# Optimization experiments

Hardware: AMD Instinct MI355X
Metric: run time of the kernel (lower is better)

The kernel has to match this reference:

```python
import jax, jax.numpy as jnp
import numpy as np

B, D_IN, D_OUT, Q_DIM = 8192, 400, 100, 10


def setup_inputs() -> dict:
    key = jax.random.key(0)
    kx, kw = jax.random.split(key)
    X = jax.random.normal(kx, (B, D_IN, Q_DIM), dtype=jnp.float32)
    # FRMap weight: randn(d_out, d_in) / sqrt(d_in)
    W = jax.random.normal(kw, (D_OUT, D_IN), dtype=jnp.float32) / (D_IN ** 0.5)
    return {"X": X, "W": W}


def reference(X, W):
    # FRMap: Y[b] = W @ X[b]  -> (B, d_out, q)
    Y = jnp.einsum('oi,biq->boq', W, X)
    # ReOrth: reduced QR of each tall-skinny (d_out, q) matrix, keep Q
    Q, _ = jnp.linalg.qr(Y, mode='reduced')  # (B, d_out, q)
    return Q
```

## Files before the change

kernel.cpp:

```cpp
#include <hip/hip_runtime.h>
#include <math.h>

#define BATCHES 8192
#define D_IN    400
#define D_OUT   100
#define QD      10
#define KT      64
#define NKT     7
#define MTILES  7
#define WFSZ    (NKT * MTILES * 2 * 64 * 8)
#define XB      648
#define NW      4

using bf16x8 = __attribute__((ext_vector_type(8))) short;
using f32x4  = __attribute__((ext_vector_type(4))) float;

template <int CTRL>
__device__ __forceinline__ float dpp_add(float x) {
  int s = __builtin_amdgcn_update_dpp(0, __builtin_bit_cast(int, x),
                                      CTRL, 0xF, 0xF, true);
  return x + __builtin_bit_cast(float, s);
}

__device__ __forceinline__ float wsum64(float x) {
  x = dpp_add<0x111>(x);
  x = dpp_add<0x112>(x);
  x = dpp_add<0x114>(x);
  x = dpp_add<0x118>(x);
  x = dpp_add<0x142>(x);
  x = dpp_add<0x143>(x);
  return __builtin_bit_cast(float,
      __builtin_amdgcn_readlane(__builtin_bit_cast(int, x), 63));
}

__device__ __forceinline__ float lane_bcast(float x, int lane) {
  return __builtin_bit_cast(float,
      __builtin_amdgcn_readlane(__builtin_bit_cast(int, x), lane));
}

__global__ __launch_bounds__(256) void wprep_kernel(const float* __restrict__ W,
                                                    short* __restrict__ wfh,
                                                    short* __restrict__ wfl) {
  const int e = blockIdx.x * 256 + threadIdx.x;
  if (e >= WFSZ) return;
  const int j = e & 7, lane = (e >> 3) & 63, ks = (e >> 9) & 1, mtkt = e >> 10;
  const int kt = mtkt / MTILES, mt = mtkt - kt * MTILES;
  const int o = mt * 16 + (lane & 15);
  const int k = kt * KT + ks * 32 + (lane >> 4) * 8 + j;
  const float w = (o < D_OUT && k < D_IN) ? W[o * D_IN + k] : 0.f;
  __bf16 h = (__bf16)w;
  float hf = (float)h;
  __bf16 l = (__bf16)(w - hf);
  wfh[e] = __builtin_bit_cast(short, h);
  wfl[e] = __builtin_bit_cast(short, l);
}


__device__ __forceinline__ void qr_and_store(const f32x4* acc, float* stg,
                                             float* dst, int lane, int col,
                                             int quad) {
  if (col < QD) {
    #pragma unroll
    for (int mt = 0; mt < MTILES; ++mt)
      #pragma unroll
      for (int rr = 0; rr < 4; ++rr) {
        const int o = mt * 16 + quad * 4 + rr;
        if (o < D_OUT) stg[o * QD + col] = acc[mt][rr];
      }
  }
  const int r = lane;
  float a0[QD], a1[QD];
  #pragma unroll
  for (int q = 0; q < QD; ++q) a0[q] = stg[r * QD + q];
  const bool has1 = (r + 64) < D_OUT;
  #pragma unroll
  for (int q = 0; q < QD; ++q) a1[q] = has1 ? stg[(r + 64) * QD + q] : 0.f;

  float v0[QD], v1[QD], tau[QD];
  #pragma unroll
  for (int j = 0; j < QD; ++j) {
    float cj0  = (r >= j) ? a0[j] : 0.f;
    float part = cj0 * cj0 + a1[j] * a1[j];
    float sig  = wsum64(part);
    float alpha = lane_bcast(a0[j], j);
    float nrm  = sqrtf(sig);
    float beta = (alpha >= 0.f) ? -nrm : nrm;
    float tj   = (nrm > 0.f) ? (beta - alpha) / beta : 0.f;
    float inv  = (nrm > 0.f) ? 1.f / (alpha - beta) : 0.f;
    tau[j] = tj;
    v0[j]  = (r == j) ? 1.f : ((r > j) ? a0[j] * inv : 0.f);
    v1[j]  = a1[j] * inv;
    #pragma unroll
    for (int k = j + 1; k < QD; ++k) {
      float p = v0[j] * a0[k] + v1[j] * a1[k];
      float s = wsum64(p) * tj;
      a0[k] -= s * v0[j];
      a1[k] -= s * v1[j];
    }
  }
  float q0[QD], q1[QD];
  #pragma unroll
  for (int c = 0; c < QD; ++c) { q0[c] = (r == c) ? 1.f : 0.f; q1[c] = 0.f; }
  #pragma unroll
  for (int j = QD - 1; j >= 0; --j) {
    #pragma unroll
    for (int c = j; c < QD; ++c) {
      float p = v0[j] * q0[c] + v1[j] * q1[c];
      float s = wsum64(p) * tau[j];
      q0[c] -= s * v0[j];
      q1[c] -= s * v1[j];
    }
  }
  #pragma unroll
  for (int c = 0; c < QD; ++c) stg[r * QD + c] = q0[c];
  if (has1) {
    #pragma unroll
    for (int c = 0; c < QD; ++c) stg[(r + 64) * QD + c] = q1[c];
  }
  const float4* src = (const float4*)stg;
  float4* d4 = (float4*)dst;
  #pragma unroll
  for (int u = r; u < (D_OUT * QD) / 4; u += 64) d4[u] = src[u];
}

__global__ __launch_bounds__(256, 3) void fused_kernel(const float* __restrict__ X,
                                                       const short* __restrict__ wfh,
                                                       const short* __restrict__ wfl,
                                                       float* __restrict__ out) {
  __shared__ float xstg[NW * 2 * XB];
  const int tid  = threadIdx.x;
  const int lane = tid & 63;
  const int wv   = __builtin_amdgcn_readfirstlane(tid >> 6);
  const long b0  = (long)blockIdx.x * (NW * 2) + wv * 2;
  float* xs = xstg + wv * (2 * XB);
  const int col = lane & 15, quad = lane >> 4;

  f32x4 acc0[MTILES], acc1[MTILES];
  #pragma unroll
  for (int t = 0; t < MTILES; ++t) {
    acc0[t] = (f32x4){0.f, 0.f, 0.f, 0.f};
    acc1[t] = (f32x4){0.f, 0.f, 0.f, 0.f};
  }

  float4 pre[5];
  #pragma unroll
  for (int u = 0; u < 5; ++u) {
    const int idx = lane + u * 64;
    const int bsel = idx >= 160 ? 1 : 0;
    const int within = idx - bsel * 160;
    pre[u] = *(const float4*)(X + (b0 + bsel) * (long)(D_IN * QD) + within * 4);
  }

  #pragma unroll 1
  for (int kt = 0; kt < NKT; ++kt) {
    const int k0 = kt * KT;
    #pragma unroll
    for (int u = 0; u < 5; ++u) {
      const int idx = lane + u * 64;
      const int bsel = idx >= 160 ? 1 : 0;
      const int within = idx - bsel * 160;
      *(float4*)&xs[bsel * XB + within * 4] = pre[u];
    }
    if (kt + 1 < NKT) {
      const int nk0 = k0 + KT;
      const int vf4 = (nk0 + KT <= D_IN) ? 160 : ((D_IN - nk0) * QD) / 4;
      #pragma unroll
      for (int u = 0; u < 5; ++u) {
        const int idx = lane + u * 64;
        const int bsel = idx >= 160 ? 1 : 0;
        const int within = idx - bsel * 160;
        float4 v = {0.f, 0.f, 0.f, 0.f};
        if (within < vf4)
          v = *(const float4*)(X + (b0 + bsel) * (long)(D_IN * QD) + nk0 * QD + within * 4);
        pre[u] = v;
      }
    }
    const short* wh_kt = wfh + (long)kt * (MTILES * 2 * 64 * 8);
    const short* wl_kt = wfl + (long)kt * (MTILES * 2 * 64 * 8);
    #pragma unroll
    for (int ks = 0; ks < 2; ++ks) {
      bf16x8 b0h, b0l, b1h, b1l;
      #pragma unroll
      for (int m = 0; m < 8; ++m) {
        const int fo = (ks * 32 + quad * 8 + m) * QD + col;
        float x0 = xs[fo];
        float x1 = xs[XB + fo];
        __bf16 h0 = (__bf16)x0; float f0 = (float)h0; __bf16 g0 = (__bf16)(x0 - f0);
        __bf16 h1 = (__bf16)x1; float f1 = (float)h1; __bf16 g1 = (__bf16)(x1 - f1);
        b0h[m] = __builtin_bit_cast(short, h0); b0l[m] = __builtin_bit_cast(short, g0);
        b1h[m] = __builtin_bit_cast(short, h1); b1l[m] = __builtin_bit_cast(short, g1);
      }
      #pragma unroll
      for (int mt = 0; mt < MTILES; ++mt) {
        const int ao = ((mt * 2 + ks) * 64 + lane) * 8;
        bf16x8 ah = *(const bf16x8*)(wh_kt + ao);
        bf16x8 al = *(const bf16x8*)(wl_kt + ao);
        acc0[mt] = __builtin_amdgcn_mfma_f32_16x16x32_bf16(ah, b0h, acc0[mt], 0, 0, 0);
        acc0[mt] = __builtin_amdgcn_mfma_f32_16x16x32_bf16(al, b0h, acc0[mt], 0, 0, 0);
        acc0[mt] = __builtin_amdgcn_mfma_f32_16x16x32_bf16(ah, b0l, acc0[mt], 0, 0, 0);
        acc1[mt] = __builtin_amdgcn_mfma_f32_16x16x32_bf16(ah, b1h, acc1[mt], 0, 0, 0);
        acc1[mt] = __builtin_amdgcn_mfma_f32_16x16x32_bf16(al, b1h, acc1[mt], 0, 0, 0);
        acc1[mt] = __builtin_amdgcn_mfma_f32_16x16x32_bf16(ah, b1l, acc1[mt], 0, 0, 0);
      }
    }
  }

  qr_and_store(acc0, xs, out + b0 * (long)(D_OUT * QD), lane, col, quad);
  qr_and_store(acc1, xs, out + (b0 + 1) * (long)(D_OUT * QD), lane, col, quad);
}

extern "C" void kernel_launch(void* const* d_in, const int* in_sizes, int n_in,
                              void* d_out, int out_size, void* d_ws, size_t ws_size,
                              hipStream_t stream) {
  const float* X = (const float*)d_in[0];
  const float* W = (const float*)d_in[1];
  float* out = (float*)d_out;
  short* wfh = (short*)d_ws;
  short* wfl = wfh + WFSZ;
  hipLaunchKernelGGL(wprep_kernel, dim3((WFSZ + 255) / 256), dim3(256), 0, stream,
                     W, wfh, wfl);
  hipLaunchKernelGGL(fused_kernel, dim3(BATCHES / (NW * 2)), dim3(256), 0, stream,
                     X, wfh, wfl, out);
}
```

Measured before the change: 272.5 us.

## Process one batch per wave and use fast rcp/sqrt in Householder QR

```diff
diff --git a/kernel.cpp b/kernel.cpp
--- a/kernel.cpp
+++ b/kernel.cpp
@@ -9,7 +9,7 @@
 #define NKT     7
 #define MTILES  7
 #define WFSZ    (NKT * MTILES * 2 * 64 * 8)
-#define XB      648
+#define XR      1008
 #define NW      4
 
 using bf16x8 = __attribute__((ext_vector_type(8))) short;
@@ -83,10 +83,13 @@
     float part = cj0 * cj0 + a1[j] * a1[j];
     float sig  = wsum64(part);
     float alpha = lane_bcast(a0[j], j);
-    float nrm  = sqrtf(sig);
-    float beta = (alpha >= 0.f) ? -nrm : nrm;
-    float tj   = (nrm > 0.f) ? (beta - alpha) / beta : 0.f;
-    float inv  = (nrm > 0.f) ? 1.f / (alpha - beta) : 0.f;
+    float nrm  = __builtin_amdgcn_sqrtf(sig);
+    float aab  = fabsf(alpha);
+    float rn   = __builtin_amdgcn_rcpf(nrm);
+    float rd   = __builtin_amdgcn_rcpf(aab + nrm);
+    float sgn  = (alpha >= 0.f) ? 1.f : -1.f;
+    float tj   = (sig > 0.f) ? (1.f + aab * rn) : 0.f;
+    float inv  = (sig > 0.f) ? sgn * rd : 0.f;
     tau[j] = tj;
     v0[j]  = (r == j) ? 1.f : ((r > j) ? a0[j] * inv : 0.f);
     v1[j]  = a1[j] * inv;
@@ -123,55 +126,48 @@
   for (int u = r; u < (D_OUT * QD) / 4; u += 64) d4[u] = src[u];
 }
 
-__global__ __launch_bounds__(256, 3) void fused_kernel(const float* __restrict__ X,
+__global__ __launch_bounds__(256, 4) void fused_kernel(const float* __restrict__ X,
                                                        const short* __restrict__ wfh,
                                                        const short* __restrict__ wfl,
                                                        float* __restrict__ out) {
-  __shared__ float xstg[NW * 2 * XB];
+  __shared__ float xstg[NW * XR];
   const int tid  = threadIdx.x;
   const int lane = tid & 63;
   const int wv   = __builtin_amdgcn_readfirstlane(tid >> 6);
-  const long b0  = (long)blockIdx.x * (NW * 2) + wv * 2;
-  float* xs = xstg + wv * (2 * XB);
+  const long b   = (long)blockIdx.x * NW + wv;
+  float* xs = xstg + wv * XR;
   const int col = lane & 15, quad = lane >> 4;
 
-  f32x4 acc0[MTILES], acc1[MTILES];
-  #pragma unroll
-  for (int t = 0; t < MTILES; ++t) {
-    acc0[t] = (f32x4){0.f, 0.f, 0.f, 0.f};
-    acc1[t] = (f32x4){0.f, 0.f, 0.f, 0.f};
-  }
-
-  float4 pre[5];
-  #pragma unroll
-  for (int u = 0; u < 5; ++u) {
+  f32x4 acc[MTILES];
+  #pragma unroll
+  for (int t = 0; t < MTILES; ++t) acc[t] = (f32x4){0.f, 0.f, 0.f, 0.f};
+
+  float4 pre[3];
+  #pragma unroll
+  for (int u = 0; u < 3; ++u) {
     const int idx = lane + u * 64;
-    const int bsel = idx >= 160 ? 1 : 0;
-    const int within = idx - bsel * 160;
-    pre[u] = *(const float4*)(X + (b0 + bsel) * (long)(D_IN * QD) + within * 4);
+    pre[u] = (float4){0.f, 0.f, 0.f, 0.f};
+    if (idx < 160)
+      pre[u] = *(const float4*)(X + b * (long)(D_IN * QD) + idx * 4);
   }
 
   #pragma unroll 1
   for (int kt = 0; kt < NKT; ++kt) {
     const int k0 = kt * KT;
     #pragma unroll
-    for (int u = 0; u < 5; ++u) {
+    for (int u = 0; u < 3; ++u) {
       const int idx = lane + u * 64;
-      const int bsel = idx >= 160 ? 1 : 0;
-      const int within = idx - bsel * 160;
-      *(float4*)&xs[bsel * XB + within * 4] = pre[u];
+      if (idx < 160) *(float4*)&xs[idx * 4] = pre[u];
     }
     if (kt + 1 < NKT) {
       const int nk0 = k0 + KT;
       const int vf4 = (nk0 + KT <= D_IN) ? 160 : ((D_IN - nk0) * QD) / 4;
       #pragma unroll
-      for (int u = 0; u < 5; ++u) {
+      for (int u = 0; u < 3; ++u) {
         const int idx = lane + u * 64;
-        const int bsel = idx >= 160 ? 1 : 0;
-        const int within = idx - bsel * 160;
         float4 v = {0.f, 0.f, 0.f, 0.f};
-        if (within < vf4)
-          v = *(const float4*)(X + (b0 + bsel) * (long)(D_IN * QD) + nk0 * QD + within * 4);
+        if (idx < vf4)
+          v = *(const float4*)(X + b * (long)(D_IN * QD) + nk0 * QD + idx * 4);
         pre[u] = v;
       }
     }
@@ -179,34 +175,28 @@
     const short* wl_kt = wfl + (long)kt * (MTILES * 2 * 64 * 8);
     #pragma unroll
     for (int ks = 0; ks < 2; ++ks) {
-      bf16x8 b0h, b0l, b1h, b1l;
+      bf16x8 bh, bl;
       #pragma unroll
       for (int m = 0; m < 8; ++m) {
         const int fo = (ks * 32 + quad * 8 + m) * QD + col;
         float x0 = xs[fo];
-        float x1 = xs[XB + fo];
         __bf16 h0 = (__bf16)x0; float f0 = (float)h0; __bf16 g0 = (__bf16)(x0 - f0);
-        __bf16 h1 = (__bf16)x1; float f1 = (float)h1; __bf16 g1 = (__bf16)(x1 - f1);
-        b0h[m] = __builtin_bit_cast(short, h0); b0l[m] = __builtin_bit_cast(short, g0);
-        b1h[m] = __builtin_bit_cast(short, h1); b1l[m] = __builtin_bit_cast(short, g1);
+        bh[m] = __builtin_bit_cast(short, h0);
+        bl[m] = __builtin_bit_cast(short, g0);
       }
       #pragma unroll
       for (int mt = 0; mt < MTILES; ++mt) {
         const int ao = ((mt * 2 + ks) * 64 + lane) * 8;
         bf16x8 ah = *(const bf16x8*)(wh_kt + ao);
         bf16x8 al = *(const bf16x8*)(wl_kt + ao);
-        acc0[mt] = __builtin_amdgcn_mfma_f32_16x16x32_bf16(ah, b0h, acc0[mt], 0, 0, 0);
-        acc0[mt] = __builtin_amdgcn_mfma_f32_16x16x32_bf16(al, b0h, acc0[mt], 0, 0, 0);
-        acc0[mt] = __builtin_amdgcn_mfma_f32_16x16x32_bf16(ah, b0l, acc0[mt], 0, 0, 0);
-        acc1[mt] = __builtin_amdgcn_mfma_f32_16x16x32_bf16(ah, b1h, acc1[mt], 0, 0, 0);
-        acc1[mt] = __builtin_amdgcn_mfma_f32_16x16x32_bf16(al, b1h, acc1[mt], 0, 0, 0);
-        acc1[mt] = __builtin_amdgcn_mfma_f32_16x16x32_bf16(ah, b1l, acc1[mt], 0, 0, 0);
-      }
-    }
-  }
-
-  qr_and_store(acc0, xs, out + b0 * (long)(D_OUT * QD), lane, col, quad);
-  qr_and_store(acc1, xs, out + (b0 + 1) * (long)(D_OUT * QD), lane, col, quad);
+        acc[mt] = __builtin_amdgcn_mfma_f32_16x16x32_bf16(ah, bh, acc[mt], 0, 0, 0);
+        acc[mt] = __builtin_amdgcn_mfma_f32_16x16x32_bf16(al, bh, acc[mt], 0, 0, 0);
+        acc[mt] = __builtin_amdgcn_mfma_f32_16x16x32_bf16(ah, bl, acc[mt], 0, 0, 0);
+      }
+    }
+  }
+
+  qr_and_store(acc, xs, out + b * (long)(D_OUT * QD), lane, col, quad);
 }
 
 extern "C" void kernel_launch(void* const* d_in, const int* in_sizes, int n_in,
@@ -219,6 +209,6 @@
   short* wfl = wfh + WFSZ;
   hipLaunchKernelGGL(wprep_kernel, dim3((WFSZ + 255) / 256), dim3(256), 0, stream,
                      W, wfh, wfl);
-  hipLaunchKernelGGL(fused_kernel, dim3(BATCHES / (NW * 2)), dim3(256), 0, stream,
+  hipLaunchKernelGGL(fused_kernel, dim3(BATCHES / NW), dim3(256), 0, stream,
                      X, wfh, wfl, out);
 }
```

New measurement: 260.6 us. 4.3% less time.

## Stage W fragments in shared memory cooperatively and use fast rcp/sqrt in QR

Applied to the files above, without the earlier changes.

```diff
diff --git a/kernel.cpp b/kernel.cpp
--- a/kernel.cpp
+++ b/kernel.cpp
@@ -11,6 +11,8 @@
 #define WFSZ    (NKT * MTILES * 2 * 64 * 8)
 #define XB      648
 #define NW      4
+#define WCH     512
+#define WHALF   (14 * WCH)
 
 using bf16x8 = __attribute__((ext_vector_type(8))) short;
 using f32x4  = __attribute__((ext_vector_type(4))) float;
@@ -36,6 +38,12 @@
 __device__ __forceinline__ float lane_bcast(float x, int lane) {
   return __builtin_bit_cast(float,
       __builtin_amdgcn_readlane(__builtin_bit_cast(int, x), lane));
+}
+
+__device__ __forceinline__ void lds_barrier() {
+  asm volatile("s_waitcnt lgkmcnt(0)" ::: "memory");
+  __builtin_amdgcn_s_barrier();
+  __builtin_amdgcn_sched_barrier(0);
 }
 
 __global__ __launch_bounds__(256) void wprep_kernel(const float* __restrict__ W,
@@ -55,7 +63,6 @@
   wfl[e] = __builtin_bit_cast(short, l);
 }
 
-
 __device__ __forceinline__ void qr_and_store(const f32x4* acc, float* stg,
                                              float* dst, int lane, int col,
                                              int quad) {
@@ -83,10 +90,13 @@
     float part = cj0 * cj0 + a1[j] * a1[j];
     float sig  = wsum64(part);
     float alpha = lane_bcast(a0[j], j);
-    float nrm  = sqrtf(sig);
-    float beta = (alpha >= 0.f) ? -nrm : nrm;
-    float tj   = (nrm > 0.f) ? (beta - alpha) / beta : 0.f;
-    float inv  = (nrm > 0.f) ? 1.f / (alpha - beta) : 0.f;
+    float nrm  = __builtin_amdgcn_sqrtf(sig);
+    float aab  = fabsf(alpha);
+    float rn   = __builtin_amdgcn_rcpf(nrm);
+    float rd   = __builtin_amdgcn_rcpf(aab + nrm);
+    float sgn  = (alpha >= 0.f) ? 1.f : -1.f;
+    float tj   = (sig > 0.f) ? (1.f + aab * rn) : 0.f;
+    float inv  = (sig > 0.f) ? sgn * rd : 0.f;
     tau[j] = tj;
     v0[j]  = (r == j) ? 1.f : ((r > j) ? a0[j] * inv : 0.f);
     v1[j]  = a1[j] * inv;
@@ -123,11 +133,12 @@
   for (int u = r; u < (D_OUT * QD) / 4; u += 64) d4[u] = src[u];
 }
 
-__global__ __launch_bounds__(256, 3) void fused_kernel(const float* __restrict__ X,
+__global__ __launch_bounds__(256, 4) void fused_kernel(const float* __restrict__ X,
                                                        const short* __restrict__ wfh,
                                                        const short* __restrict__ wfl,
                                                        float* __restrict__ out) {
-  __shared__ float xstg[NW * 2 * XB];
+  __shared__ __align__(16) float xstg[NW * 2 * XB];
+  __shared__ __align__(16) short wtile[WHALF];
   const int tid  = threadIdx.x;
   const int lane = tid & 63;
   const int wv   = __builtin_amdgcn_readfirstlane(tid >> 6);
@@ -142,18 +153,42 @@
     acc1[t] = (f32x4){0.f, 0.f, 0.f, 0.f};
   }
 
+  bf16x8 wst[4];
+  auto wload = [&](int kt, int ks) {
+    #pragma unroll
+    for (int i = 0; i < 4; ++i) {
+      const int c = wv + 4 * i;
+      if (c < 14) {
+        const short* pl = (c < 7) ? wfh : wfl;
+        const int m = (c < 7) ? c : c - 7;
+        wst[i] = *(const bf16x8*)(pl + ((long)(kt * 7 + m) * 2 + ks) * WCH + lane * 8);
+      }
+    }
+  };
+  auto wcommit = [&]() {
+    #pragma unroll
+    for (int i = 0; i < 4; ++i) {
+      const int c = wv + 4 * i;
+      if (c < 14) *(bf16x8*)&wtile[c * WCH + lane * 8] = wst[i];
+    }
+  };
+
   float4 pre[5];
-  #pragma unroll
-  for (int u = 0; u < 5; ++u) {
-    const int idx = lane + u * 64;
-    const int bsel = idx >= 160 ? 1 : 0;
-    const int within = idx - bsel * 160;
-    pre[u] = *(const float4*)(X + (b0 + bsel) * (long)(D_IN * QD) + within * 4);
-  }
-
-  #pragma unroll 1
-  for (int kt = 0; kt < NKT; ++kt) {
-    const int k0 = kt * KT;
+  auto xpre = [&](int kt) {
+    const int nk0 = kt * KT;
+    const int vf4 = (nk0 + KT <= D_IN) ? 160 : ((D_IN - nk0) * QD) / 4;
+    #pragma unroll
+    for (int u = 0; u < 5; ++u) {
+      const int idx = lane + u * 64;
+      const int bsel = idx >= 160 ? 1 : 0;
+      const int within = idx - bsel * 160;
+      float4 v = {0.f, 0.f, 0.f, 0.f};
+      if (within < vf4)
+        v = *(const float4*)(X + (b0 + bsel) * (long)(D_IN * QD) + nk0 * QD + within * 4);
+      pre[u] = v;
+    }
+  };
+  auto xcommit = [&]() {
     #pragma unroll
     for (int u = 0; u < 5; ++u) {
       const int idx = lane + u * 64;
@@ -161,48 +196,52 @@
       const int within = idx - bsel * 160;
       *(float4*)&xs[bsel * XB + within * 4] = pre[u];
     }
-    if (kt + 1 < NKT) {
-      const int nk0 = k0 + KT;
-      const int vf4 = (nk0 + KT <= D_IN) ? 160 : ((D_IN - nk0) * QD) / 4;
-      #pragma unroll
-      for (int u = 0; u < 5; ++u) {
-        const int idx = lane + u * 64;
-        const int bsel = idx >= 160 ? 1 : 0;
-        const int within = idx - bsel * 160;
-        float4 v = {0.f, 0.f, 0.f, 0.f};
-        if (within < vf4)
-          v = *(const float4*)(X + (b0 + bsel) * (long)(D_IN * QD) + nk0 * QD + within * 4);
-        pre[u] = v;
-      }
-    }
-    const short* wh_kt = wfh + (long)kt * (MTILES * 2 * 64 * 8);
-    const short* wl_kt = wfl + (long)kt * (MTILES * 2 * 64 * 8);
-    #pragma unroll
-    for (int ks = 0; ks < 2; ++ks) {
-      bf16x8 b0h, b0l, b1h, b1l;
-      #pragma unroll
-      for (int m = 0; m < 8; ++m) {
-        const int fo = (ks * 32 + quad * 8 + m) * QD + col;
-        float x0 = xs[fo];
-        float x1 = xs[XB + fo];
-        __bf16 h0 = (__bf16)x0; float f0 = (float)h0; __bf16 g0 = (__bf16)(x0 - f0);
-        __bf16 h1 = (__bf16)x1; float f1 = (float)h1; __bf16 g1 = (__bf16)(x1 - f1);
-        b0h[m] = __builtin_bit_cast(short, h0); b0l[m] = __builtin_bit_cast(short, g0);
-        b1h[m] = __builtin_bit_cast(short, h1); b1l[m] = __builtin_bit_cast(short, g1);
-      }
-      #pragma unroll
-      for (int mt = 0; mt < MTILES; ++mt) {
-        const int ao = ((mt * 2 + ks) * 64 + lane) * 8;
-        bf16x8 ah = *(const bf16x8*)(wh_kt + ao);
-        bf16x8 al = *(const bf16x8*)(wl_kt + ao);
-        acc0[mt] = __builtin_amdgcn_mfma_f32_16x16x32_bf16(ah, b0h, acc0[mt], 0, 0, 0);
-        acc0[mt] = __builtin_amdgcn_mfma_f32_16x16x32_bf16(al, b0h, acc0[mt], 0, 0, 0);
-        acc0[mt] = __builtin_amdgcn_mfma_f32_16x16x32_bf16(ah, b0l, acc0[mt], 0, 0, 0);
-        acc1[mt] = __builtin_amdgcn_mfma_f32_16x16x32_bf16(ah, b1h, acc1[mt], 0, 0, 0);
-        acc1[mt] = __builtin_amdgcn_mfma_f32_16x16x32_bf16(al, b1h, acc1[mt], 0, 0, 0);
-        acc1[mt] = __builtin_amdgcn_mfma_f32_16x16x32_bf16(ah, b1l, acc1[mt], 0, 0, 0);
-      }
-    }
+  };
+
+  auto computeHalf = [&](int ks) {
+    bf16x8 b0h, b0l, b1h, b1l;
+    #pragma unroll
+    for (int m = 0; m < 8; ++m) {
+      const int fo = (ks * 32 + quad * 8 + m) * QD + col;
+      float x0 = xs[fo];
+      float x1 = xs[XB + fo];
+      __bf16 h0 = (__bf16)x0; float f0 = (float)h0; __bf16 g0 = (__bf16)(x0 - f0);
+      __bf16 h1 = (__bf16)x1; float f1 = (float)h1; __bf16 g1 = (__bf16)(x1 - f1);
+      b0h[m] = __builtin_bit_cast(short, h0); b0l[m] = __builtin_bit_cast(short, g0);
+      b1h[m] = __builtin_bit_cast(short, h1); b1l[m] = __builtin_bit_cast(short, g1);
+    }
+    #pragma unroll
+    for (int mt = 0; mt < MTILES; ++mt) {
+      bf16x8 ah = *(const bf16x8*)&wtile[mt * WCH + lane * 8];
+      bf16x8 al = *(const bf16x8*)&wtile[(7 + mt) * WCH + lane * 8];
+      acc0[mt] = __builtin_amdgcn_mfma_f32_16x16x32_bf16(ah, b0h, acc0[mt], 0, 0, 0);
+      acc0[mt] = __builtin_amdgcn_mfma_f32_16x16x32_bf16(al, b0h, acc0[mt], 0, 0, 0);
+      acc0[mt] = __builtin_amdgcn_mfma_f32_16x16x32_bf16(ah, b0l, acc0[mt], 0, 0, 0);
+      acc1[mt] = __builtin_amdgcn_mfma_f32_16x16x32_bf16(ah, b1h, acc1[mt], 0, 0, 0);
+      acc1[mt] = __builtin_amdgcn_mfma_f32_16x16x32_bf16(al, b1h, acc1[mt], 0, 0, 0);
+      acc1[mt] = __builtin_amdgcn_mfma_f32_16x16x32_bf16(ah, b1l, acc1[mt], 0, 0, 0);
+    }
+  };
+
+  wload(0, 0);
+  xpre(0);
+  wcommit();
+  lds_barrier();
+
+  #pragma unroll 1
+  for (int kt = 0; kt < NKT; ++kt) {
+    wload(kt, 1);
+    xcommit();
+    if (kt + 1 < NKT) xpre(kt + 1);
+    computeHalf(0);
+    lds_barrier();
+    wcommit();
+    lds_barrier();
+    if (kt + 1 < NKT) wload(kt + 1, 0);
+    computeHalf(1);
+    lds_barrier();
+    if (kt + 1 < NKT) wcommit();
+    lds_barrier();
   }
 
   qr_and_store(acc0, xs, out + b0 * (long)(D_OUT * QD), lane, col, quad);
```

Result: no change. 273.7 us (+0.4%).
